# Performance work log

Measured on AMD Instinct MI355X. Metric: run time of the kernel, lower is better.

## Reference

```python
import jax, jax.numpy as jnp
import numpy as np

# dims
B, L, H, W, C = 1, 5, 100, 176, 256   # batch, agents, BEV height, BEV width, channels
HEADS, DHEAD, T = 8, 32, 3            # heads, per-head dim, num agent types
D = HEADS * DHEAD                     # == C here (to_qkv inner dim)
SCALE = DHEAD ** -0.5


def setup_inputs() -> dict:
    key = jax.random.key(0)
    ks = jax.random.split(key, 14)
    x = jax.random.normal(ks[0], (B, L, H, W, C), jnp.float32)
    mask = jnp.ones((B, H, W, 1, L), jnp.int32)
    types = jax.random.randint(ks[1], (B, L), 0, T)
    # prior_encoding: [B, L, 1, 1, 3] = (velocity, dt, type); only type (channel 2) is used
    prior_encoding = jnp.zeros((B, L, 1, 1, 3), jnp.float32).at[..., 2].set(
        types[:, :, None, None].astype(jnp.float32))
    s = C ** -0.5
    Wq = jax.random.normal(ks[2], (T, C, D), jnp.float32) * s
    bq = jax.random.normal(ks[3], (T, D), jnp.float32) * 0.01
    Wk = jax.random.normal(ks[4], (T, C, D), jnp.float32) * s
    bk = jax.random.normal(ks[5], (T, D), jnp.float32) * 0.01
    Wv = jax.random.normal(ks[6], (T, C, D), jnp.float32) * s
    bv = jax.random.normal(ks[7], (T, D), jnp.float32) * 0.01
    Wa = jax.random.normal(ks[8], (T, D, C), jnp.float32) * (D ** -0.5)
    ba = jax.random.normal(ks[9], (T, C), jnp.float32) * 0.01
    rel_att = jax.random.normal(ks[10], (T * T, HEADS, DHEAD, DHEAD), jnp.float32) * (DHEAD ** -0.5)
    rel_msg = jax.random.normal(ks[11], (T * T, HEADS, DHEAD, DHEAD), jnp.float32) * (DHEAD ** -0.5)
    return dict(x=x, mask=mask, prior_encoding=prior_encoding,
                Wq=Wq, bq=bq, Wk=Wk, bk=bk, Wv=Wv, bv=bv, Wa=Wa, ba=ba,
                rel_att=rel_att, rel_msg=rel_msg)


def _split_heads(t):
    # [B,H,W,L,D] -> [B,m,H,W,L,p]
    return jnp.transpose(t.reshape(B, H, W, L, HEADS, DHEAD), (0, 4, 1, 2, 3, 5))


def reference(x, mask, prior_encoding, Wq, bq, Wk, bk, Wv, bv, Wa, ba, rel_att, rel_msg):
    types = prior_encoding[:, :, 0, 0, 2].astype(jnp.int32)      # [B,L]
    xp = jnp.transpose(x, (0, 2, 3, 1, 4))                        # [B,H,W,L,C]

    def proj(Wt, bt):
        # per-agent-type linear: gather weights per agent, then batched matmul
        return jnp.einsum('bhwlc,blcd->bhwld', xp, Wt[types]) + bt[types][:, None, None]

    q = _split_heads(proj(Wq, bq))                                # [B,m,H,W,L,p]
    k = _split_heads(proj(Wk, bk))
    v = _split_heads(proj(Wv, bv))

    etype = types[:, :, None] * T + types[:, None, :]             # [B,L,L]
    w_att = jnp.transpose(rel_att[etype], (0, 3, 1, 2, 4, 5))     # [B,m,L,L,p,q]
    w_msg = jnp.transpose(rel_msg[etype], (0, 3, 1, 2, 4, 5))     # [B,m,L,L,p,c]

    att = jnp.einsum('bmhwip,bmijpq,bmhwjq->bmhwij', q, w_att, k) * SCALE
    att = jnp.where(mask[:, None] == 0, -jnp.inf, att)            # mask [B,1,H,W,1,L]
    att = jax.nn.softmax(att, axis=-1)

    v_msg = jnp.einsum('bmijpc,bmhwjp->bmhwijc', w_msg, v)        # relation-weighted messages
    out = jnp.einsum('bmhwij,bmhwijc->bmhwic', att, v_msg)        # [B,m,H,W,L,c]

    out = jnp.transpose(out, (0, 2, 3, 4, 1, 5)).reshape(B, H, W, L, D)
    out = jnp.einsum('bhwld,bldc->bhwlc', out, Wa[types]) + ba[types][:, None, None]
    return jnp.transpose(out, (0, 3, 1, 2, 4))                    # [B,L,H,W,C]
```

## Files before the change

### kernel.cpp

```cpp
#include <hip/hip_runtime.h>
#include <math.h>

#define HW     17600
#define CD     256
#define LAG    5
#define NHEAD  8
#define DH     32
#define NT     3

typedef short bf16x8 __attribute__((ext_vector_type(8)));
typedef float f32x4  __attribute__((ext_vector_type(4)));

__device__ __forceinline__ float bflo(unsigned u) { return __uint_as_float(u << 16); }
__device__ __forceinline__ float bfhi(unsigned u) { return __uint_as_float(u & 0xffff0000u); }
__device__ __forceinline__ unsigned f2bf(float f) {
    unsigned u = __float_as_uint(f);
    return (u + 0x7fffu + ((u >> 16) & 1u)) >> 16;
}
__device__ __forceinline__ unsigned pack2(float a, float b) {
    return f2bf(a) | (f2bf(b) << 16);
}

typedef __attribute__((address_space(1))) const unsigned int gu32;
typedef __attribute__((address_space(3))) unsigned int       lu32;
__device__ __forceinline__ void gload_lds16(const void* g, void* l) {
    __builtin_amdgcn_global_load_lds(
        (gu32*)(unsigned long long)(uintptr_t)g,
        (lu32*)(unsigned int)(uintptr_t)l, 16, 0, 0);
}

__global__ __launch_bounds__(256) void convert_w_kernel(
    const float* __restrict__ Wq, const float* __restrict__ Wk,
    const float* __restrict__ Wv, const float* __restrict__ Wa,
    unsigned short* __restrict__ Wt)
{
    __shared__ float tile[64][65];
    const int mat = blockIdx.y;
    const int k0 = (blockIdx.x >> 2) * 64;
    const int n0 = (blockIdx.x & 3) * 64;
    const float* W;
    if      (mat < 3) W = Wq + (long)mat * 65536;
    else if (mat < 6) W = Wk + (long)(mat - 3) * 65536;
    else if (mat < 9) W = Wv + (long)(mat - 6) * 65536;
    else              W = Wa + (long)(mat - 9) * 65536;
    const int t = threadIdx.x;
#pragma unroll
    for (int r = 0; r < 16; ++r) {
        int idx = r * 256 + t;
        int row = idx >> 6, col = idx & 63;
        tile[row][col] = W[(long)(k0 + row) * 256 + n0 + col];
    }
    __syncthreads();
    unsigned short* dst = Wt + (long)mat * 65536;
#pragma unroll
    for (int r = 0; r < 16; ++r) {
        int idx = r * 256 + t;
        int row = idx >> 6, col = idx & 63;
        dst[(long)(n0 + row) * 256 + k0 + col] = (unsigned short)f2bf(tile[col][row]);
    }
}

__global__ __launch_bounds__(256) void convert_rel_kernel(
    const float* __restrict__ rel_att, const float* __restrict__ rel_msg,
    unsigned short* __restrict__ rattT, unsigned short* __restrict__ rmsgT)
{
    const long base = ((long)(blockIdx.x * NHEAD + blockIdx.y)) << 10;
    const int t = threadIdx.x;
#pragma unroll
    for (int i = 0; i < 4; ++i) {
        int idx = t * 4 + i;
        int p = idx >> 5, q = idx & 31;
        rattT[base + q * 32 + p] = (unsigned short)f2bf(rel_att[base + idx]);
        rmsgT[base + q * 32 + p] = (unsigned short)f2bf(rel_msg[base + idx]);
    }
}

template<bool AF32, bool YBF>
__device__ __forceinline__ void gemm_mfma_core(
    const void* __restrict__ Aptr, long lda,
    const unsigned short* __restrict__ Wt,
    const float* __restrict__ bias,
    void* __restrict__ Yptr, long ldy)
{
    __shared__ unsigned short As[64 * 64];
    __shared__ unsigned short Ws[256 * 64];

    const int t  = threadIdx.x;
    const int m0 = blockIdx.x * 64;
    const int w  = t >> 6;
    const int l  = t & 63;
    const int wr = w >> 1;
    const int wc = w & 1;
    const int fr = l & 15;
    const int ko = (l >> 4) << 3;

    const int srow = t >> 3;
    const int colu = (t & 7) << 3;
    const int axor = (fr & 7) << 3;

    f32x4 acc[2][8];
#pragma unroll
    for (int i = 0; i < 2; ++i)
#pragma unroll
        for (int j = 0; j < 8; ++j) {
            acc[i][j][0] = 0.f; acc[i][j][1] = 0.f;
            acc[i][j][2] = 0.f; acc[i][j][3] = 0.f;
        }

    for (int ks = 0; ks < 4; ++ks) {
        const int k0 = ks << 6;
        __syncthreads();
#pragma unroll
        for (int r = 0; r < 2; ++r) {
            const int row  = r * 32 + srow;
            const int xr   = (row & 7) << 3;
            const int scol = colu ^ xr;
            if (AF32) {
                const float* src = (const float*)Aptr + (long)(m0 + row) * lda + k0 + colu;
                float4 f0 = *(const float4*)src;
                float4 f1 = *(const float4*)(src + 4);
                uint4 u;
                u.x = pack2(f0.x, f0.y); u.y = pack2(f0.z, f0.w);
                u.z = pack2(f1.x, f1.y); u.w = pack2(f1.z, f1.w);
                *(uint4*)(&As[row * 64 + scol]) = u;
            } else {
                const unsigned short* src =
                    (const unsigned short*)Aptr + (long)(m0 + row) * lda + k0 + scol;
                gload_lds16(src, &As[r * 2048 + w * 512]);
            }
        }
#pragma unroll
        for (int r = 0; r < 8; ++r) {
            const int row  = r * 32 + srow;
            const int scol = colu ^ ((row & 7) << 3);
            const unsigned short* src = Wt + (long)row * 256 + k0 + scol;
            gload_lds16(src, &Ws[r * 2048 + w * 512]);
        }
        __syncthreads();
#pragma unroll
        for (int kk = 0; kk < 2; ++kk) {
            const int fcol = ((kk << 5) | ko) ^ axor;
            bf16x8 a[2], b[8];
#pragma unroll
            for (int i = 0; i < 2; ++i)
                a[i] = *(const bf16x8*)(&As[(wr * 32 + i * 16 + fr) * 64 + fcol]);
#pragma unroll
            for (int j = 0; j < 8; ++j)
                b[j] = *(const bf16x8*)(&Ws[(wc * 128 + j * 16 + fr) * 64 + fcol]);
#pragma unroll
            for (int i = 0; i < 2; ++i)
#pragma unroll
                for (int j = 0; j < 8; ++j)
                    acc[i][j] = __builtin_amdgcn_mfma_f32_16x16x32_bf16(
                        a[i], b[j], acc[i][j], 0, 0, 0);
        }
    }

    const int fq = l >> 4;
#pragma unroll
    for (int j = 0; j < 8; ++j) {
        int col = wc * 128 + j * 16 + fr;
        float bz = bias[col];
#pragma unroll
        for (int i = 0; i < 2; ++i) {
            int rowb = m0 + wr * 32 + i * 16 + (fq << 2);
#pragma unroll
            for (int e = 0; e < 4; ++e) {
                float v = acc[i][j][e] + bz;
                if (YBF)
                    ((unsigned short*)Yptr)[(long)(rowb + e) * ldy + col] =
                        (unsigned short)f2bf(v);
                else
                    ((float*)Yptr)[(long)(rowb + e) * ldy + col] = v;
            }
        }
    }
}

__global__ __launch_bounds__(256) void gemm_qkv_mfma(
    const float* __restrict__ x, const float* __restrict__ pe,
    const unsigned short* __restrict__ Wt,
    const float* __restrict__ bq, const float* __restrict__ bk,
    const float* __restrict__ bv,
    unsigned short* __restrict__ qws, unsigned short* __restrict__ kws,
    unsigned short* __restrict__ vws)
{
    const int lag = blockIdx.z;
    const int tpe = (int)pe[lag * 3 + 2];
    const float* A = x + (long)lag * HW * CD;

#pragma unroll 1
    for (int proj = 0; proj < 3; ++proj) {
        const unsigned short* Wm = Wt + (long)(proj * 3 + tpe) * 65536;
        const float* bias;
        unsigned short* Y;
        long ldy;
        if      (proj == 0) { bias = bq; Y = qws + (long)lag * CD; ldy = LAG * CD; }
        else if (proj == 1) { bias = bk; Y = kws + (long)lag * HW * CD; ldy = CD; }
        else                { bias = bv; Y = vws + (long)lag * HW * CD; ldy = CD; }
        bias += tpe * CD;
        gemm_mfma_core<true, true>(A, CD, Wm, bias, Y, ldy);
        __syncthreads();
    }
}

__global__ __launch_bounds__(256) void gemm_out_mfma(
    const unsigned short* __restrict__ aws, const float* __restrict__ pe,
    const unsigned short* __restrict__ Wt, const float* __restrict__ ba,
    float* __restrict__ out)
{
    const int lag = blockIdx.z;
    const int tpe = (int)pe[lag * 3 + 2];
    const unsigned short* A = aws + (long)lag * CD;
    const unsigned short* Wm = Wt + (long)(9 + tpe) * 65536;
    const float* bias = ba + tpe * CD;
    float* Y = out + (long)lag * HW * CD;
    gemm_mfma_core<false, false>(A, (long)LAG * CD, Wm, bias, Y, CD);
}

#define QTROW 488

__global__ __launch_bounds__(256) void attn_fused_kernel(
    const unsigned short* __restrict__ qws,
    const unsigned short* __restrict__ kws,
    const unsigned short* __restrict__ vws,
    const unsigned short* __restrict__ rattT,
    const unsigned short* __restrict__ rmsgT,
    const int* __restrict__ mask, const float* __restrict__ pe,
    unsigned short* __restrict__ aws)
{
    __shared__ unsigned short lds[4 * 16 * QTROW];

    const int t    = threadIdx.x;
    const int w    = t >> 6;
    const int l    = t & 63;
    const int fr   = l & 15;
    const int fq   = l >> 4;
    const int m    = blockIdx.y;
    const int pix0 = blockIdx.x * 64;

    const int pl2   = t >> 2;
    const int sub   = t & 3;
    const int gpix2 = pix0 + pl2;

    int ty[LAG];
#pragma unroll
    for (int i = 0; i < LAG; ++i) ty[i] = (int)pe[i * 3 + 2];
    bool pres[NT] = {false, false, false};
#pragma unroll
    for (int i = 0; i < LAG; ++i) {
        pres[0] = pres[0] || (ty[i] == 0);
        pres[1] = pres[1] || (ty[i] == 1);
        pres[2] = pres[2] || (ty[i] == 2);
    }

    uint4 kf[LAG], vf[LAG];
    int mk[LAG];
#pragma unroll
    for (int j = 0; j < LAG; ++j) {
        const long off = ((long)j * HW + gpix2) * CD + m * DH + sub * 8;
        kf[j] = *(const uint4*)(kws + off);
        vf[j] = *(const uint4*)(vws + off);
        mk[j] = mask[gpix2 * LAG + j];
    }

    {
        bf16x8 aq[LAG];
#pragma unroll
        for (int i = 0; i < LAG; ++i)
            aq[i] = *(const bf16x8*)(qws + (long)(pix0 + w * 16 + fr) * (LAG * CD)
                                     + i * CD + m * DH + fq * 8);
        const int qtbase = w * 16 * QTROW;
#pragma unroll
        for (int sg = 0; sg < NT; ++sg) {
            if (!pres[sg]) continue;
#pragma unroll
            for (int i = 0; i < LAG; ++i) {
                const int e = ty[i] * NT + sg;
                const unsigned short* bb = rattT + ((long)(e * NHEAD + m) << 10);
                bf16x8 b0 = *(const bf16x8*)(bb + fr * 32 + fq * 8);
                bf16x8 b1 = *(const bf16x8*)(bb + (fr + 16) * 32 + fq * 8);
                f32x4 z = {0.f, 0.f, 0.f, 0.f};
                f32x4 d0 = __builtin_amdgcn_mfma_f32_16x16x32_bf16(aq[i], b0, z, 0, 0, 0);
                f32x4 d1 = __builtin_amdgcn_mfma_f32_16x16x32_bf16(aq[i], b1, z, 0, 0, 0);
#pragma unroll
                for (int e4 = 0; e4 < 4; ++e4) {
                    const int idx = qtbase + (fq * 4 + e4) * QTROW + (i * NT + sg) * 32;
                    lds[idx + fr]      = (unsigned short)f2bf(d0[e4]);
                    lds[idx + fr + 16] = (unsigned short)f2bf(d1[e4]);
                }
            }
        }
    }
    __syncthreads();

    const float scale = 0.17677669529663687f;
    float att[LAG][LAG];
    {
        const int qtb = w * 16 * QTROW + (pl2 & 15) * QTROW;
#pragma unroll
        for (int j = 0; j < LAG; ++j) {
            float kx[8];
            kx[0] = bflo(kf[j].x); kx[1] = bfhi(kf[j].x);
            kx[2] = bflo(kf[j].y); kx[3] = bfhi(kf[j].y);
            kx[4] = bflo(kf[j].z); kx[5] = bfhi(kf[j].z);
            kx[6] = bflo(kf[j].w); kx[7] = bfhi(kf[j].w);
            const int tyj = ty[j];
#pragma unroll
            for (int i = 0; i < LAG; ++i) {
                uint4 qv = *(const uint4*)(&lds[qtb + (i * NT + tyj) * 32 + sub * 8]);
                float part;
                part = bflo(qv.x) * kx[0];
                part = fmaf(bfhi(qv.x), kx[1], part);
                part = fmaf(bflo(qv.y), kx[2], part);
                part = fmaf(bfhi(qv.y), kx[3], part);
                part = fmaf(bflo(qv.z), kx[4], part);
                part = fmaf(bfhi(qv.z), kx[5], part);
                part = fmaf(bflo(qv.w), kx[6], part);
                part = fmaf(bfhi(qv.w), kx[7], part);
                part += __shfl_xor(part, 1);
                part += __shfl_xor(part, 2);
                att[i][j] = part * scale;
            }
        }
#pragma unroll
        for (int i = 0; i < LAG; ++i) {
            float mx = -INFINITY;
#pragma unroll
            for (int j = 0; j < LAG; ++j) {
                att[i][j] = mk[j] ? att[i][j] : -INFINITY;
                mx = fmaxf(mx, att[i][j]);
            }
            float ssum = 0.f;
#pragma unroll
            for (int j = 0; j < LAG; ++j) {
                att[i][j] = __expf(att[i][j] - mx);
                ssum += att[i][j];
            }
            float inv = 1.f / ssum;
#pragma unroll
            for (int j = 0; j < LAG; ++j) att[i][j] *= inv;
        }
    }

    float vx[LAG][8];
#pragma unroll
    for (int j = 0; j < LAG; ++j) {
        vx[j][0] = bflo(vf[j].x); vx[j][1] = bfhi(vf[j].x);
        vx[j][2] = bflo(vf[j].y); vx[j][3] = bfhi(vf[j].y);
        vx[j][4] = bflo(vf[j].z); vx[j][5] = bfhi(vf[j].z);
        vx[j][6] = bflo(vf[j].w); vx[j][7] = bfhi(vf[j].w);
    }

    f32x4 oacc[LAG][2];
#pragma unroll
    for (int i = 0; i < LAG; ++i)
#pragma unroll
        for (int c = 0; c < 2; ++c) {
            oacc[i][c][0] = 0.f; oacc[i][c][1] = 0.f;
            oacc[i][c][2] = 0.f; oacc[i][c][3] = 0.f;
        }

    const int baddr = (((l & 15) << 2) | (l >> 4)) << 2;

#pragma unroll
    for (int sg = 0; sg < NT; ++sg) {
        if (!pres[sg]) continue;
#pragma unroll
        for (int i = 0; i < LAG; ++i) {
            float vg[8] = {0.f,0.f,0.f,0.f,0.f,0.f,0.f,0.f};
#pragma unroll
            for (int j = 0; j < LAG; ++j) {
                float wj = (ty[j] == sg) ? att[i][j] : 0.f;
#pragma unroll
                for (int d = 0; d < 8; ++d) vg[d] = fmaf(wj, vx[j][d], vg[d]);
            }
            int p0 = (int)pack2(vg[0], vg[1]);
            int p1 = (int)pack2(vg[2], vg[3]);
            int p2 = (int)pack2(vg[4], vg[5]);
            int p3 = (int)pack2(vg[6], vg[7]);
            int r0 = __builtin_amdgcn_ds_bpermute(baddr, p0);
            int r1 = __builtin_amdgcn_ds_bpermute(baddr, p1);
            int r2 = __builtin_amdgcn_ds_bpermute(baddr, p2);
            int r3 = __builtin_amdgcn_ds_bpermute(baddr, p3);
            int av[4] = {r0, r1, r2, r3};
            bf16x8 a = *(const bf16x8*)av;

            const int e = ty[i] * NT + sg;
            const unsigned short* bb = rmsgT + ((long)(e * NHEAD + m) << 10);
            bf16x8 b0 = *(const bf16x8*)(bb + fr * 32 + fq * 8);
            bf16x8 b1 = *(const bf16x8*)(bb + (fr + 16) * 32 + fq * 8);
            oacc[i][0] = __builtin_amdgcn_mfma_f32_16x16x32_bf16(a, b0, oacc[i][0], 0, 0, 0);
            oacc[i][1] = __builtin_amdgcn_mfma_f32_16x16x32_bf16(a, b1, oacc[i][1], 0, 0, 0);
        }
    }

#pragma unroll
    for (int i = 0; i < LAG; ++i) {
#pragma unroll
        for (int e4 = 0; e4 < 4; ++e4) {
            const long ob = (long)(pix0 + w * 16 + fq * 4 + e4) * (LAG * CD)
                            + i * CD + m * DH;
            aws[ob + fr]      = (unsigned short)f2bf(oacc[i][0][e4]);
            aws[ob + fr + 16] = (unsigned short)f2bf(oacc[i][1][e4]);
        }
    }
}

extern "C" void kernel_launch(void* const* d_in, const int* in_sizes, int n_in,
                              void* d_out, int out_size, void* d_ws, size_t ws_size,
                              hipStream_t stream) {
    const float* x    = (const float*)d_in[0];
    const int*   mask = (const int*)  d_in[1];
    const float* pe   = (const float*)d_in[2];
    const float* Wq   = (const float*)d_in[3];
    const float* bq   = (const float*)d_in[4];
    const float* Wk   = (const float*)d_in[5];
    const float* bk   = (const float*)d_in[6];
    const float* Wv   = (const float*)d_in[7];
    const float* bv   = (const float*)d_in[8];
    const float* Wa   = (const float*)d_in[9];
    const float* ba   = (const float*)d_in[10];
    const float* ratt = (const float*)d_in[11];
    const float* rmsg = (const float*)d_in[12];
    float* out = (float*)d_out;

    const size_t PLANE = (size_t)LAG * HW * CD;

    unsigned short* qws   = (unsigned short*)d_ws;
    unsigned short* kws   = qws + PLANE;
    unsigned short* vws   = kws + PLANE;
    unsigned short* aws   = vws + PLANE;
    unsigned short* Wt    = aws + PLANE;
    unsigned short* rattT = Wt + 786432;
    unsigned short* rmsgT = rattT + 73728;

    convert_w_kernel<<<dim3(16, 12), 256, 0, stream>>>(Wq, Wk, Wv, Wa, Wt);
    convert_rel_kernel<<<dim3(9, 8), 256, 0, stream>>>(ratt, rmsg, rattT, rmsgT);

    gemm_qkv_mfma<<<dim3(HW / 64, 1, LAG), 256, 0, stream>>>(
        x, pe, Wt, bq, bk, bv, qws, kws, vws);

    attn_fused_kernel<<<dim3(HW / 64, NHEAD), 256, 0, stream>>>(
        qws, kws, vws, rattT, rmsgT, mask, pe, aws);

    gemm_out_mfma<<<dim3(HW / 64, 1, LAG), 256, 0, stream>>>(aws, pe, Wt, ba, out);
}
```

Baseline: 193.4 us.

## Stage full A tile in LDS once and read weights directly from global

The GEMM core now loads the whole 64x256 activation tile into LDS once per block, before any compute. In the QKV kernel that single converted tile is shared by all three projections instead of being reloaded three times. Weight fragments are now read straight from global memory (relying on L1/L2 cache) instead of being staged through a 256x64 LDS buffer each k-step, which removes the per-k-step barriers. The risk is higher global load latency for the weights, now read without swizzled LDS reuse, which could stall the MFMA loop.

```diff
diff --git a/kernel.cpp b/kernel.cpp
--- a/kernel.cpp
+++ b/kernel.cpp
@@ -75,27 +75,19 @@
     }
 }
 
-template<bool AF32, bool YBF>
-__device__ __forceinline__ void gemm_mfma_core(
-    const void* __restrict__ Aptr, long lda,
-    const unsigned short* __restrict__ Wt,
+__device__ __forceinline__ void gemm_compute_v2(
+    const unsigned short* __restrict__ As,
+    const unsigned short* __restrict__ Wm,
     const float* __restrict__ bias,
-    void* __restrict__ Yptr, long ldy)
-{
-    __shared__ unsigned short As[64 * 64];
-    __shared__ unsigned short Ws[256 * 64];
-
+    void* __restrict__ Yptr, long ldy, int m0, bool ybf)
+{
     const int t  = threadIdx.x;
-    const int m0 = blockIdx.x * 64;
     const int w  = t >> 6;
     const int l  = t & 63;
     const int wr = w >> 1;
     const int wc = w & 1;
     const int fr = l & 15;
     const int ko = (l >> 4) << 3;
-
-    const int srow = t >> 3;
-    const int colu = (t & 7) << 3;
     const int axor = (fr & 7) << 3;
 
     f32x4 acc[2][8];
@@ -108,45 +100,17 @@
         }
 
     for (int ks = 0; ks < 4; ++ks) {
-        const int k0 = ks << 6;
-        __syncthreads();
-#pragma unroll
-        for (int r = 0; r < 2; ++r) {
-            const int row  = r * 32 + srow;
-            const int xr   = (row & 7) << 3;
-            const int scol = colu ^ xr;
-            if (AF32) {
-                const float* src = (const float*)Aptr + (long)(m0 + row) * lda + k0 + colu;
-                float4 f0 = *(const float4*)src;
-                float4 f1 = *(const float4*)(src + 4);
-                uint4 u;
-                u.x = pack2(f0.x, f0.y); u.y = pack2(f0.z, f0.w);
-                u.z = pack2(f1.x, f1.y); u.w = pack2(f1.z, f1.w);
-                *(uint4*)(&As[row * 64 + scol]) = u;
-            } else {
-                const unsigned short* src =
-                    (const unsigned short*)Aptr + (long)(m0 + row) * lda + k0 + scol;
-                gload_lds16(src, &As[r * 2048 + w * 512]);
-            }
-        }
-#pragma unroll
-        for (int r = 0; r < 8; ++r) {
-            const int row  = r * 32 + srow;
-            const int scol = colu ^ ((row & 7) << 3);
-            const unsigned short* src = Wt + (long)row * 256 + k0 + scol;
-            gload_lds16(src, &Ws[r * 2048 + w * 512]);
-        }
-        __syncthreads();
 #pragma unroll
         for (int kk = 0; kk < 2; ++kk) {
-            const int fcol = ((kk << 5) | ko) ^ axor;
+            const int kbase = (ks << 6) | (kk << 5) | ko;
+            const int fcol  = (ks << 6) | (((kk << 5) | ko) ^ axor);
             bf16x8 a[2], b[8];
 #pragma unroll
+            for (int j = 0; j < 8; ++j)
+                b[j] = *(const bf16x8*)(Wm + (long)(wc * 128 + j * 16 + fr) * 256 + kbase);
+#pragma unroll
             for (int i = 0; i < 2; ++i)
-                a[i] = *(const bf16x8*)(&As[(wr * 32 + i * 16 + fr) * 64 + fcol]);
-#pragma unroll
-            for (int j = 0; j < 8; ++j)
-                b[j] = *(const bf16x8*)(&Ws[(wc * 128 + j * 16 + fr) * 64 + fcol]);
+                a[i] = *(const bf16x8*)(&As[(wr * 32 + i * 16 + fr) * 256 + fcol]);
 #pragma unroll
             for (int i = 0; i < 2; ++i)
 #pragma unroll
@@ -167,7 +131,7 @@
 #pragma unroll
             for (int e = 0; e < 4; ++e) {
                 float v = acc[i][j][e] + bz;
-                if (YBF)
+                if (ybf)
                     ((unsigned short*)Yptr)[(long)(rowb + e) * ldy + col] =
                         (unsigned short)f2bf(v);
                 else
@@ -185,9 +149,29 @@
     unsigned short* __restrict__ qws, unsigned short* __restrict__ kws,
     unsigned short* __restrict__ vws)
 {
+    __shared__ unsigned short As[64 * 256];
+
+    const int t   = threadIdx.x;
+    const int m0  = blockIdx.x * 64;
     const int lag = blockIdx.z;
     const int tpe = (int)pe[lag * 3 + 2];
     const float* A = x + (long)lag * HW * CD;
+
+#pragma unroll
+    for (int r = 0; r < 8; ++r) {
+        int idx  = r * 256 + t;
+        int row  = idx >> 5;
+        int colg = (idx & 31) << 3;
+        int scol = colg ^ ((row & 7) << 3);
+        const float* src = A + (long)(m0 + row) * CD + colg;
+        float4 f0 = *(const float4*)src;
+        float4 f1 = *(const float4*)(src + 4);
+        uint4 u;
+        u.x = pack2(f0.x, f0.y); u.y = pack2(f0.z, f0.w);
+        u.z = pack2(f1.x, f1.y); u.w = pack2(f1.z, f1.w);
+        *(uint4*)(&As[row * 256 + scol]) = u;
+    }
+    __syncthreads();
 
 #pragma unroll 1
     for (int proj = 0; proj < 3; ++proj) {
@@ -199,8 +183,7 @@
         else if (proj == 1) { bias = bk; Y = kws + (long)lag * HW * CD; ldy = CD; }
         else                { bias = bv; Y = vws + (long)lag * HW * CD; ldy = CD; }
         bias += tpe * CD;
-        gemm_mfma_core<true, true>(A, CD, Wm, bias, Y, ldy);
-        __syncthreads();
+        gemm_compute_v2(As, Wm, bias, Y, ldy, m0, true);
     }
 }
 
@@ -209,13 +192,29 @@
     const unsigned short* __restrict__ Wt, const float* __restrict__ ba,
     float* __restrict__ out)
 {
+    __shared__ unsigned short As[64 * 256];
+
+    const int t   = threadIdx.x;
+    const int m0  = blockIdx.x * 64;
     const int lag = blockIdx.z;
     const int tpe = (int)pe[lag * 3 + 2];
     const unsigned short* A = aws + (long)lag * CD;
+
+#pragma unroll
+    for (int r = 0; r < 8; ++r) {
+        int idx  = r * 256 + t;
+        int row  = idx >> 5;
+        int colg = (idx & 31) << 3;
+        int scol = colg ^ ((row & 7) << 3);
+        const unsigned short* src = A + (long)(m0 + row) * (LAG * CD) + scol;
+        gload_lds16(src, &As[idx * 8]);
+    }
+    __syncthreads();
+
     const unsigned short* Wm = Wt + (long)(9 + tpe) * 65536;
     const float* bias = ba + tpe * CD;
     float* Y = out + (long)lag * HW * CD;
-    gemm_mfma_core<false, false>(A, (long)LAG * CD, Wm, bias, Y, CD);
+    gemm_compute_v2(As, Wm, bias, Y, CD, m0, false);
 }
 
 #define QTROW 488
```

After: 305.3 us. 57.8% more time.
